# Optimization experiments

Measured on AMD Instinct MI355X. Metric: run time of the kernel, lower is better.

Reference implementation:

```python
import jax, jax.numpy as jnp
import numpy as np

N_NODES = 50000
N_EDGES = 800000
IN_DIM = 128
OUT_DIM = 128


def setup_inputs() -> dict:
    key = jax.random.key(0)
    k1, k2, k3, k4, k5, k6 = jax.random.split(key, 6)
    X = jax.random.normal(k1, (N_NODES, IN_DIM), dtype=jnp.float32)
    src = jax.random.randint(k2, (N_EDGES,), 0, N_NODES, dtype=jnp.int32)
    dst = jax.random.randint(k3, (N_EDGES,), 0, N_NODES, dtype=jnp.int32)
    # nn.Linear(in, out, bias=False) weight has shape (out, in)
    lim = 1.0 / np.sqrt(IN_DIM)
    W_self = jax.random.uniform(k4, (OUT_DIM, IN_DIM), dtype=jnp.float32, minval=-lim, maxval=lim)
    W_neigh = jax.random.uniform(k5, (OUT_DIM, IN_DIM), dtype=jnp.float32, minval=-lim, maxval=lim)
    bias = jnp.zeros((OUT_DIM,), dtype=jnp.float32)
    return {"X": X, "src": src, "dst": dst, "W_self": W_self, "W_neigh": W_neigh, "bias": bias}


def reference(X, src, dst, W_self, W_neigh, bias):
    # h_u = ReLU( W_self x_u + sum_{(v->u) in E} W_neigh x_v + bias )
    # Transform once per node (n_nodes x in_dim x out_dim GEMMs), then
    # gather transformed source features and scatter-add into destinations.
    h_self = jnp.einsum('ni,oi->no', X, W_self)        # [N, out]
    xw_neigh = jnp.einsum('ni,oi->no', X, W_neigh)     # [N, out]
    h_neigh = jax.ops.segment_sum(xw_neigh[src], dst, num_segments=N_NODES)
    return jax.nn.relu(h_self + h_neigh + bias)
```

## Files before the change

### kernel.cpp

```cpp
#include <hip/hip_runtime.h>

#define IN_DIM 128
#define OUT_DIM 128
#define BM 64
#define KT 32

typedef __attribute__((ext_vector_type(8))) short short8v;
typedef __attribute__((ext_vector_type(4))) float float4v;

__device__ __forceinline__ unsigned short bf16_hi(float x) {
    unsigned int u = __float_as_uint(x);
    return (unsigned short)((u + 0x7fffu + ((u >> 16) & 1u)) >> 16);
}
__device__ __forceinline__ float bf16_tof(unsigned short h) {
    return __uint_as_float(((unsigned int)h) << 16);
}

__global__ void scatter_kernel(const float* __restrict__ X,
                               const int* __restrict__ src,
                               const int* __restrict__ dst,
                               float* __restrict__ A,
                               int n_edges) {
    int gtid = blockIdx.x * blockDim.x + threadIdx.x;
    int e = gtid >> 5;
    if (e >= n_edges) return;
    int sub = gtid & 31;
    int s = src[e];
    int d = dst[e];
    const float4 v = *reinterpret_cast<const float4*>(
        X + (size_t)s * IN_DIM + sub * 4);
    float* o = A + (size_t)d * IN_DIM + sub * 4;
    unsafeAtomicAdd(o + 0, v.x);
    unsafeAtomicAdd(o + 1, v.y);
    unsafeAtomicAdd(o + 2, v.z);
    unsafeAtomicAdd(o + 3, v.w);
}

__global__ void hist_kernel(const int* __restrict__ dst, int* __restrict__ counts,
                            int n_edges) {
    int i = blockIdx.x * blockDim.x + threadIdx.x;
    int e0 = i * 4;
    if (e0 + 4 <= n_edges) {
        int4 d4 = *reinterpret_cast<const int4*>(dst + e0);
        atomicAdd(&counts[d4.x], 1);
        atomicAdd(&counts[d4.y], 1);
        atomicAdd(&counts[d4.z], 1);
        atomicAdd(&counts[d4.w], 1);
    } else {
        for (int e = e0; e < n_edges; ++e) atomicAdd(&counts[dst[e]], 1);
    }
}

__global__ __launch_bounds__(256)
void scan1_kernel(const int* __restrict__ counts, int* __restrict__ offs,
                  int* __restrict__ bsums, int n) {
    __shared__ int tmp[256];
    const int tid = threadIdx.x;
    const int i = blockIdx.x * 256 + tid;
    const int v = (i < n) ? counts[i] : 0;
    tmp[tid] = v;
    __syncthreads();
    #pragma unroll
    for (int d = 1; d < 256; d <<= 1) {
        int t = (tid >= d) ? tmp[tid - d] : 0;
        __syncthreads();
        tmp[tid] += t;
        __syncthreads();
    }
    if (i < n) offs[i] = tmp[tid] - v;
    if (tid == 255) bsums[blockIdx.x] = tmp[255];
}

__global__ __launch_bounds__(256)
void scan2_kernel(int* __restrict__ bsums, int nb) {
    __shared__ int tmp[256];
    __shared__ int carry;
    const int tid = threadIdx.x;
    if (tid == 0) carry = 0;
    __syncthreads();
    for (int base = 0; base < nb; base += 256) {
        const int i = base + tid;
        const int v = (i < nb) ? bsums[i] : 0;
        tmp[tid] = v;
        __syncthreads();
        #pragma unroll
        for (int d = 1; d < 256; d <<= 1) {
            int t = (tid >= d) ? tmp[tid - d] : 0;
            __syncthreads();
            tmp[tid] += t;
            __syncthreads();
        }
        if (i < nb) bsums[i] = carry + tmp[tid] - v;
        __syncthreads();
        if (tid == 0) carry += tmp[255];
        __syncthreads();
    }
}

__global__ __launch_bounds__(256)
void scan3_kernel(int* __restrict__ offs, const int* __restrict__ bsums,
                  int* __restrict__ cursor, int n) {
    const int i = blockIdx.x * 256 + threadIdx.x;
    if (i < n) {
        const int o = offs[i] + bsums[blockIdx.x];
        offs[i] = o;
        cursor[i] = o;
    }
}

__global__ void bucket_kernel(const int* __restrict__ src,
                              const int* __restrict__ dst,
                              int* __restrict__ cursor,
                              int* __restrict__ src_sorted, int n_edges) {
    int e = blockIdx.x * blockDim.x + threadIdx.x;
    if (e < n_edges) {
        const int pos = atomicAdd(&cursor[dst[e]], 1);
        src_sorted[pos] = src[e];
    }
}

__global__ __launch_bounds__(256)
void accum_split_kernel(const float* __restrict__ X,
                        const int* __restrict__ offs,
                        const int* __restrict__ src_sorted,
                        unsigned short* __restrict__ Ahi,
                        unsigned short* __restrict__ Alo,
                        int n_nodes, int n_edges) {
    const int tid = threadIdx.x;
    const int u = blockIdx.x * 8 + (tid >> 5);
    if (u >= n_nodes) return;
    const int sub = tid & 31;

    const int beg = offs[u];
    const int end = (u == n_nodes - 1) ? n_edges : offs[u + 1];

    float4 acc = make_float4(0.f, 0.f, 0.f, 0.f);
    int e = beg;
    for (; e + 4 <= end; e += 4) {
        const int s0 = src_sorted[e + 0];
        const int s1 = src_sorted[e + 1];
        const int s2 = src_sorted[e + 2];
        const int s3 = src_sorted[e + 3];
        const float4 v0 = *reinterpret_cast<const float4*>(X + (size_t)s0 * IN_DIM + sub * 4);
        const float4 v1 = *reinterpret_cast<const float4*>(X + (size_t)s1 * IN_DIM + sub * 4);
        const float4 v2 = *reinterpret_cast<const float4*>(X + (size_t)s2 * IN_DIM + sub * 4);
        const float4 v3 = *reinterpret_cast<const float4*>(X + (size_t)s3 * IN_DIM + sub * 4);
        acc.x += v0.x + v1.x + v2.x + v3.x;
        acc.y += v0.y + v1.y + v2.y + v3.y;
        acc.z += v0.z + v1.z + v2.z + v3.z;
        acc.w += v0.w + v1.w + v2.w + v3.w;
    }
    for (; e < end; ++e) {
        const int s = src_sorted[e];
        const float4 v = *reinterpret_cast<const float4*>(X + (size_t)s * IN_DIM + sub * 4);
        acc.x += v.x; acc.y += v.y; acc.z += v.z; acc.w += v.w;
    }

    ushort4 hi, lo;
    hi.x = bf16_hi(acc.x); lo.x = bf16_hi(acc.x - bf16_tof(hi.x));
    hi.y = bf16_hi(acc.y); lo.y = bf16_hi(acc.y - bf16_tof(hi.y));
    hi.z = bf16_hi(acc.z); lo.z = bf16_hi(acc.z - bf16_tof(hi.z));
    hi.w = bf16_hi(acc.w); lo.w = bf16_hi(acc.w - bf16_tof(hi.w));
    *reinterpret_cast<ushort4*>(Ahi + (size_t)u * IN_DIM + sub * 4) = hi;
    *reinterpret_cast<ushort4*>(Alo + (size_t)u * IN_DIM + sub * 4) = lo;
}

__global__ void xsplit_kernel(const float* __restrict__ X,
                              unsigned short* __restrict__ Xsp, int n_nodes) {
    int i = blockIdx.x * blockDim.x + threadIdx.x;
    if (i >= n_nodes * 32) return;
    const int node = i >> 5, g = i & 31;
    const float4 x = *reinterpret_cast<const float4*>(X + (size_t)node * IN_DIM + g * 4);
    ushort4 hi, lo;
    hi.x = bf16_hi(x.x); lo.x = bf16_hi(x.x - bf16_tof(hi.x));
    hi.y = bf16_hi(x.y); lo.y = bf16_hi(x.y - bf16_tof(hi.y));
    hi.z = bf16_hi(x.z); lo.z = bf16_hi(x.z - bf16_tof(hi.z));
    hi.w = bf16_hi(x.w); lo.w = bf16_hi(x.w - bf16_tof(hi.w));
    *reinterpret_cast<ushort4*>(Xsp + (size_t)node * 256 + g * 4) = hi;
    *reinterpret_cast<ushort4*>(Xsp + (size_t)node * 256 + 128 + g * 4) = lo;
}

__global__ void wsplit_kernel(const float* __restrict__ W1,
                              const float* __restrict__ W2,
                              unsigned short* __restrict__ W1h,
                              unsigned short* __restrict__ W1l,
                              unsigned short* __restrict__ W2h,
                              unsigned short* __restrict__ W2l) {
    int i = blockIdx.x * blockDim.x + threadIdx.x;
    if (i >= OUT_DIM * IN_DIM) return;
    float a = W1[i], b = W2[i];
    unsigned short ah = bf16_hi(a), bh = bf16_hi(b);
    W1h[i] = ah; W1l[i] = bf16_hi(a - bf16_tof(ah));
    W2h[i] = bh; W2l[i] = bf16_hi(b - bf16_tof(bh));
}

__global__ __launch_bounds__(256, 4)
void mfma_gemm_kernel(const unsigned short* Xsp,
                      const unsigned short* __restrict__ Ahi,
                      const unsigned short* __restrict__ Alo,
                      const unsigned short* __restrict__ W1h,
                      const unsigned short* __restrict__ W1l,
                      const unsigned short* __restrict__ W2h,
                      const unsigned short* __restrict__ W2l,
                      const float* __restrict__ bias,
                      float* out,
                      int n_nodes) {
    __shared__ unsigned short Fs[64 * 64];
    __shared__ unsigned short Ws[128 * 64];

    const int tid  = threadIdx.x;
    const int lane = tid & 63;
    const int wid  = tid >> 6;
    const int wm   = wid >> 1;
    const int wn   = wid & 1;
    const int lr   = lane & 15;
    const int lk   = lane >> 4;
    const int node0 = blockIdx.x * 64;

    const int fr = tid >> 3;
    const int c  = tid & 7;
    const int swz = (c ^ (fr & 7)) * 8;

    float4v acc[2][4];
    #pragma unroll
    for (int mi = 0; mi < 2; ++mi)
        #pragma unroll
        for (int ni = 0; ni < 4; ++ni) acc[mi][ni] = (float4v)0.f;

    const unsigned short* wseg[6] = {W1h, W1l, W1h, W2h, W2l, W2h};

    short8v fv[2], wv[4];

    {
        const int seg = 0, khalf = 0;
        #pragma unroll
        for (int j = 0; j < 2; ++j) {
            const int node = node0 + fr + j * 32;
            short8v v = (short8v)0;
            if (node < n_nodes)
                v = *reinterpret_cast<const short8v*>(
                    Xsp + (size_t)node * 256 + khalf + c * 8);
            fv[j] = v;
        }
        #pragma unroll
        for (int j = 0; j < 4; ++j)
            wv[j] = *reinterpret_cast<const short8v*>(
                wseg[seg] + (size_t)(fr + j * 32) * 128 + khalf + c * 8);
    }

    #pragma unroll
    for (int t = 0; t < 12; ++t) {
        __syncthreads();
        #pragma unroll
        for (int j = 0; j < 2; ++j)
            *reinterpret_cast<short8v*>(&Fs[(fr + j * 32) * 64 + swz]) = fv[j];
        #pragma unroll
        for (int j = 0; j < 4; ++j)
            *reinterpret_cast<short8v*>(&Ws[(fr + j * 32) * 64 + swz]) = wv[j];
        __syncthreads();

        if (t < 11) {
            const int tn = t + 1;
            const int seg = tn >> 1;
            const int khalf = (tn & 1) * 64;
            #pragma unroll
            for (int j = 0; j < 2; ++j) {
                const int node = node0 + fr + j * 32;
                short8v v = (short8v)0;
                if (node < n_nodes) {
                    if (seg < 3) {
                        v = *reinterpret_cast<const short8v*>(
                            Xsp + (size_t)node * 256 + (seg == 2 ? 128 : 0) +
                            khalf + c * 8);
                    } else {
                        const unsigned short* Ap = (seg == 5) ? Alo : Ahi;
                        v = *reinterpret_cast<const short8v*>(
                            Ap + (size_t)node * 128 + khalf + c * 8);
                    }
                }
                fv[j] = v;
            }
            #pragma unroll
            for (int j = 0; j < 4; ++j)
                wv[j] = *reinterpret_cast<const short8v*>(
                    wseg[seg] + (size_t)(fr + j * 32) * 128 + khalf + c * 8);
        }

        #pragma unroll
        for (int ks = 0; ks < 2; ++ks) {
            const int cc = ((ks * 4 + lk) ^ (lr & 7)) * 8;
            short8v a[2], b[4];
            #pragma unroll
            for (int mi = 0; mi < 2; ++mi) {
                const int row = wm * 32 + mi * 16 + lr;
                a[mi] = *reinterpret_cast<const short8v*>(&Fs[row * 64 + cc]);
            }
            #pragma unroll
            for (int ni = 0; ni < 4; ++ni) {
                const int o = wn * 64 + ni * 16 + lr;
                b[ni] = *reinterpret_cast<const short8v*>(&Ws[o * 64 + cc]);
            }
            #pragma unroll
            for (int mi = 0; mi < 2; ++mi)
                #pragma unroll
                for (int ni = 0; ni < 4; ++ni)
                    acc[mi][ni] = __builtin_amdgcn_mfma_f32_16x16x32_bf16(
                        a[mi], b[ni], acc[mi][ni], 0, 0, 0);
        }
    }

    #pragma unroll
    for (int ni = 0; ni < 4; ++ni) {
        const int o = wn * 64 + ni * 16 + lr;
        const float bo = bias[o];
        #pragma unroll
        for (int mi = 0; mi < 2; ++mi) {
            const int nodeb = node0 + wm * 32 + mi * 16 + lk * 4;
            #pragma unroll
            for (int r = 0; r < 4; ++r) {
                const int node = nodeb + r;
                if (node < n_nodes)
                    out[(size_t)node * OUT_DIM + o] =
                        fmaxf(acc[mi][ni][r] + bo, 0.f);
            }
        }
    }
}

__global__ __launch_bounds__(256)
void gemm_kernel(const float* __restrict__ X,
                 const float* __restrict__ A,
                 const float* __restrict__ Wself,
                 const float* __restrict__ Wneigh,
                 const float* __restrict__ bias,
                 float* __restrict__ out,
                 int n_nodes) {
    __shared__ alignas(16) float Wt[KT][132];
    __shared__ alignas(16) float Xs[BM][KT + 4];

    const int tid   = threadIdx.x;
    const int o_grp = tid & 31;
    const int n_grp = tid >> 5;
    const int node0 = blockIdx.x * BM;

    float acc[8][4];
    #pragma unroll
    for (int i = 0; i < 8; ++i)
        #pragma unroll
        for (int j = 0; j < 4; ++j) acc[i][j] = 0.f;

    for (int kt = 0; kt < 2 * IN_DIM; kt += KT) {
        const float* Wsrc = (kt < IN_DIM) ? Wself : Wneigh;
        const float* Fsrc = (kt < IN_DIM) ? X : A;
        const int kbase = kt & (IN_DIM - 1);
        __syncthreads();
        {
            const int k4 = tid & 7;
            int o = tid >> 3;
            #pragma unroll
            for (int p = 0; p < 4; ++p, o += 32) {
                float4 w = *reinterpret_cast<const float4*>(
                    Wsrc + o * IN_DIM + kbase + k4 * 4);
                Wt[k4 * 4 + 0][o] = w.x;
                Wt[k4 * 4 + 1][o] = w.y;
                Wt[k4 * 4 + 2][o] = w.z;
                Wt[k4 * 4 + 3][o] = w.w;
            }
        }
        {
            const int k4 = tid & 7;
            int n = tid >> 3;
            #pragma unroll
            for (int p = 0; p < 2; ++p, n += 32) {
                const int node = node0 + n;
                float4 x = make_float4(0.f, 0.f, 0.f, 0.f);
                if (node < n_nodes)
                    x = *reinterpret_cast<const float4*>(
                        Fsrc + (size_t)node * IN_DIM + kbase + k4 * 4);
                *reinterpret_cast<float4*>(&Xs[n][k4 * 4]) = x;
            }
        }
        __syncthreads();
        #pragma unroll
        for (int k4 = 0; k4 < KT; k4 += 4) {
            float4 w0 = *reinterpret_cast<const float4*>(&Wt[k4 + 0][o_grp * 4]);
            float4 w1 = *reinterpret_cast<const float4*>(&Wt[k4 + 1][o_grp * 4]);
            float4 w2 = *reinterpret_cast<const float4*>(&Wt[k4 + 2][o_grp * 4]);
            float4 w3 = *reinterpret_cast<const float4*>(&Wt[k4 + 3][o_grp * 4]);
            #pragma unroll
            for (int nn = 0; nn < 8; ++nn) {
                float4 x = *reinterpret_cast<const float4*>(
                    &Xs[n_grp * 8 + nn][k4]);
                acc[nn][0] = fmaf(x.x, w0.x, acc[nn][0]);
                acc[nn][0] = fmaf(x.y, w1.x, acc[nn][0]);
                acc[nn][0] = fmaf(x.z, w2.x, acc[nn][0]);
                acc[nn][0] = fmaf(x.w, w3.x, acc[nn][0]);
                acc[nn][1] = fmaf(x.x, w0.y, acc[nn][1]);
                acc[nn][1] = fmaf(x.y, w1.y, acc[nn][1]);
                acc[nn][1] = fmaf(x.z, w2.y, acc[nn][1]);
                acc[nn][1] = fmaf(x.w, w3.y, acc[nn][1]);
                acc[nn][2] = fmaf(x.x, w0.z, acc[nn][2]);
                acc[nn][2] = fmaf(x.y, w1.z, acc[nn][2]);
                acc[nn][2] = fmaf(x.z, w2.z, acc[nn][2]);
                acc[nn][2] = fmaf(x.w, w3.z, acc[nn][2]);
                acc[nn][3] = fmaf(x.x, w0.w, acc[nn][3]);
                acc[nn][3] = fmaf(x.y, w1.w, acc[nn][3]);
                acc[nn][3] = fmaf(x.z, w2.w, acc[nn][3]);
                acc[nn][3] = fmaf(x.w, w3.w, acc[nn][3]);
            }
        }
    }

    const float4 b = *reinterpret_cast<const float4*>(bias + o_grp * 4);
    #pragma unroll
    for (int nn = 0; nn < 8; ++nn) {
        const int node = node0 + n_grp * 8 + nn;
        if (node < n_nodes) {
            float4 r;
            r.x = fmaxf(acc[nn][0] + b.x, 0.f);
            r.y = fmaxf(acc[nn][1] + b.y, 0.f);
            r.z = fmaxf(acc[nn][2] + b.z, 0.f);
            r.w = fmaxf(acc[nn][3] + b.w, 0.f);
            *reinterpret_cast<float4*>(
                out + (size_t)node * OUT_DIM + o_grp * 4) = r;
        }
    }
}

extern "C" void kernel_launch(void* const* d_in, const int* in_sizes, int n_in,
                              void* d_out, int out_size, void* d_ws, size_t ws_size,
                              hipStream_t stream) {
    const float* X      = (const float*)d_in[0];
    const int*   src    = (const int*)d_in[1];
    const int*   dst    = (const int*)d_in[2];
    const float* Wself  = (const float*)d_in[3];
    const float* Wneigh = (const float*)d_in[4];
    const float* bias   = (const float*)d_in[5];
    float*       out    = (float*)d_out;

    const int n_nodes = in_sizes[0] / IN_DIM;
    const int n_edges = in_sizes[1];
    const int nb = (n_nodes + 255) / 256;

    char* w = (char*)d_ws;
    auto take = [&](size_t bytes) {
        char* p = w;
        w += (bytes + 15) & ~(size_t)15;
        return p;
    };
    unsigned short* Ahi = (unsigned short*)take((size_t)n_nodes * IN_DIM * 2);
    unsigned short* Alo = (unsigned short*)take((size_t)n_nodes * IN_DIM * 2);
    int* counts    = (int*)take((size_t)n_nodes * sizeof(int));
    int* offs      = (int*)take((size_t)n_nodes * sizeof(int));
    int* cursor    = (int*)take((size_t)n_nodes * sizeof(int));
    int* bsums     = (int*)take((size_t)nb * sizeof(int));
    int* srcsorted = (int*)take((size_t)n_edges * sizeof(int));
    unsigned short* W1h = (unsigned short*)take((size_t)OUT_DIM * IN_DIM * 2);
    unsigned short* W1l = (unsigned short*)take((size_t)OUT_DIM * IN_DIM * 2);
    unsigned short* W2h = (unsigned short*)take((size_t)OUT_DIM * IN_DIM * 2);
    unsigned short* W2l = (unsigned short*)take((size_t)OUT_DIM * IN_DIM * 2);
    const size_t needed = (size_t)(w - (char*)d_ws);

    const int eblocks = (n_edges + 255) / 256;

    if (needed <= ws_size) {
        hipMemsetAsync(counts, 0, (size_t)n_nodes * sizeof(int), stream);
        hist_kernel<<<(n_edges / 4 + 256) / 256 + 1, 256, 0, stream>>>(dst, counts, n_edges);
        scan1_kernel<<<nb, 256, 0, stream>>>(counts, offs, bsums, n_nodes);
        scan2_kernel<<<1, 256, 0, stream>>>(bsums, nb);
        scan3_kernel<<<nb, 256, 0, stream>>>(offs, bsums, cursor, n_nodes);
        bucket_kernel<<<eblocks, 256, 0, stream>>>(src, dst, cursor, srcsorted,
                                                   n_edges);
        unsigned short* Xsp = (unsigned short*)d_out;
        xsplit_kernel<<<(n_nodes * 32 + 255) / 256, 256, 0, stream>>>(X, Xsp, n_nodes);
        wsplit_kernel<<<(OUT_DIM * IN_DIM + 255) / 256, 256, 0, stream>>>(
            Wself, Wneigh, W1h, W1l, W2h, W2l);
        accum_split_kernel<<<(n_nodes + 7) / 8, 256, 0, stream>>>(
            X, offs, srcsorted, Ahi, Alo, n_nodes, n_edges);
        mfma_gemm_kernel<<<(n_nodes + 63) / 64, 256, 0, stream>>>(
            Xsp, Ahi, Alo, W1h, W1l, W2h, W2l, bias, out, n_nodes);
    } else {
        float* A = (float*)d_ws;
        hipMemsetAsync(A, 0, (size_t)n_nodes * IN_DIM * sizeof(float), stream);
        const long long sthreads = (long long)n_edges * 32;
        const int sblocks = (int)((sthreads + 255) / 256);
        scatter_kernel<<<sblocks, 256, 0, stream>>>(X, src, dst, A, n_edges);
        gemm_kernel<<<(n_nodes + BM - 1) / BM, 256, 0, stream>>>(
            X, A, Wself, Wneigh, bias, out, n_nodes);
    }
}
```

Measured before the change: 264.4 us.

## Fuse CSR build and neighbor aggregation into one cooperative persistent kernel

Merges the preprocessing pipeline into a single cooperatively launched persistent kernel separated by grid-wide syncs. It covers zeroing counts, splitting the weights and X into bf16 hi/lo, the histogram, the three-pass scan, bucketing by destination and the neighbor accumulation. This removes many separate kernel launches and the memset on the stream. The accumulation loop is also unrolled to eight edges with two accumulators for more memory-level parallelism. In exchange it relies on cooperative launch, pays for several grid.sync barriers, and runs the serial block-sum scan on one block while the rest of the grid waits; a multi-kernel fallback is kept.

```diff
diff --git a/kernel.cpp b/kernel.cpp
--- a/kernel.cpp
+++ b/kernel.cpp
@@ -1,4 +1,7 @@
 #include <hip/hip_runtime.h>
+#include <hip/hip_cooperative_groups.h>
+
+namespace cg = cooperative_groups;
 
 #define IN_DIM 128
 #define OUT_DIM 128
@@ -7,6 +10,7 @@
 
 typedef __attribute__((ext_vector_type(8))) short short8v;
 typedef __attribute__((ext_vector_type(4))) float float4v;
+typedef __attribute__((ext_vector_type(4))) float f4v;
 
 __device__ __forceinline__ unsigned short bf16_hi(float x) {
     unsigned int u = __float_as_uint(x);
@@ -14,6 +18,495 @@
 }
 __device__ __forceinline__ float bf16_tof(unsigned short h) {
     return __uint_as_float(((unsigned int)h) << 16);
+}
+
+__global__ __launch_bounds__(256, 4)
+void fused_all_kernel(const float* __restrict__ X,
+                      const int* __restrict__ src,
+                      const int* __restrict__ dst,
+                      const float* __restrict__ Wself,
+                      const float* __restrict__ Wneigh,
+                      int* __restrict__ counts,
+                      int* __restrict__ offs,
+                      int* __restrict__ cursor,
+                      int* __restrict__ bsums,
+                      int* __restrict__ srcsorted,
+                      unsigned short* __restrict__ Ahi,
+                      unsigned short* __restrict__ Alo,
+                      unsigned short* __restrict__ W1h,
+                      unsigned short* __restrict__ W1l,
+                      unsigned short* __restrict__ W2h,
+                      unsigned short* __restrict__ W2l,
+                      unsigned short* __restrict__ Xsp,
+                      int n_nodes, int n_edges, int nb) {
+    cg::grid_group grid = cg::this_grid();
+    __shared__ int tmp[256];
+    __shared__ int carry;
+
+    const int tid   = threadIdx.x;
+    const int gsize = gridDim.x * 256;
+    const int gtid  = blockIdx.x * 256 + tid;
+
+    for (int i = gtid; i < n_nodes; i += gsize) counts[i] = 0;
+    for (int i = gtid; i < OUT_DIM * IN_DIM; i += gsize) {
+        float a = Wself[i], b = Wneigh[i];
+        unsigned short ah = bf16_hi(a), bh = bf16_hi(b);
+        W1h[i] = ah; W1l[i] = bf16_hi(a - bf16_tof(ah));
+        W2h[i] = bh; W2l[i] = bf16_hi(b - bf16_tof(bh));
+    }
+    for (int i = gtid; i < n_nodes * 32; i += gsize) {
+        const int node = i >> 5, g = i & 31;
+        const float4 x = *reinterpret_cast<const float4*>(
+            X + (size_t)node * IN_DIM + g * 4);
+        ushort4 hi, lo;
+        hi.x = bf16_hi(x.x); lo.x = bf16_hi(x.x - bf16_tof(hi.x));
+        hi.y = bf16_hi(x.y); lo.y = bf16_hi(x.y - bf16_tof(hi.y));
+        hi.z = bf16_hi(x.z); lo.z = bf16_hi(x.z - bf16_tof(hi.z));
+        hi.w = bf16_hi(x.w); lo.w = bf16_hi(x.w - bf16_tof(hi.w));
+        *reinterpret_cast<ushort4*>(Xsp + (size_t)node * 256 + g * 4) = hi;
+        *reinterpret_cast<ushort4*>(Xsp + (size_t)node * 256 + 128 + g * 4) = lo;
+    }
+    grid.sync();
+
+    {
+        const int n4 = n_edges >> 2;
+        for (int i = gtid; i < n4; i += gsize) {
+            int4 d4 = reinterpret_cast<const int4*>(dst)[i];
+            atomicAdd(&counts[d4.x], 1);
+            atomicAdd(&counts[d4.y], 1);
+            atomicAdd(&counts[d4.z], 1);
+            atomicAdd(&counts[d4.w], 1);
+        }
+        for (int e = (n4 << 2) + gtid; e < n_edges; e += gsize)
+            atomicAdd(&counts[dst[e]], 1);
+    }
+    grid.sync();
+
+    for (int ci = blockIdx.x; ci < nb; ci += gridDim.x) {
+        const int i = ci * 256 + tid;
+        const int v = (i < n_nodes) ? counts[i] : 0;
+        tmp[tid] = v;
+        __syncthreads();
+        #pragma unroll
+        for (int d = 1; d < 256; d <<= 1) {
+            int t = (tid >= d) ? tmp[tid - d] : 0;
+            __syncthreads();
+            tmp[tid] += t;
+            __syncthreads();
+        }
+        if (i < n_nodes) offs[i] = tmp[tid] - v;
+        if (tid == 255) bsums[ci] = tmp[255];
+        __syncthreads();
+    }
+    grid.sync();
+
+    if (blockIdx.x == 0) {
+        if (tid == 0) carry = 0;
+        __syncthreads();
+        for (int base = 0; base < nb; base += 256) {
+            const int i = base + tid;
+            const int v = (i < nb) ? bsums[i] : 0;
+            tmp[tid] = v;
+            __syncthreads();
+            #pragma unroll
+            for (int d = 1; d < 256; d <<= 1) {
+                int t = (tid >= d) ? tmp[tid - d] : 0;
+                __syncthreads();
+                tmp[tid] += t;
+                __syncthreads();
+            }
+            if (i < nb) bsums[i] = carry + tmp[tid] - v;
+            __syncthreads();
+            if (tid == 0) carry += tmp[255];
+            __syncthreads();
+        }
+    }
+    grid.sync();
+
+    for (int i = gtid; i < n_nodes; i += gsize) {
+        const int o = offs[i] + bsums[i >> 8];
+        offs[i] = o;
+        cursor[i] = o;
+    }
+    grid.sync();
+
+    for (int e = gtid; e < n_edges; e += gsize) {
+        const int pos = atomicAdd(&cursor[dst[e]], 1);
+        srcsorted[pos] = src[e];
+    }
+    grid.sync();
+
+    {
+        const int sub  = tid & 31;
+        const int grp  = gtid >> 5;
+        const int ngrp = gsize >> 5;
+        for (int u = grp; u < n_nodes; u += ngrp) {
+            const int beg = offs[u];
+            const int end = (u == n_nodes - 1) ? n_edges : offs[u + 1];
+            f4v a0 = (f4v)0.f, a1 = (f4v)0.f;
+            int e = beg;
+            for (; e + 8 <= end; e += 8) {
+                const int s0 = srcsorted[e + 0];
+                const int s1 = srcsorted[e + 1];
+                const int s2 = srcsorted[e + 2];
+                const int s3 = srcsorted[e + 3];
+                const int s4 = srcsorted[e + 4];
+                const int s5 = srcsorted[e + 5];
+                const int s6 = srcsorted[e + 6];
+                const int s7 = srcsorted[e + 7];
+                f4v v0 = *reinterpret_cast<const f4v*>(X + (size_t)s0 * IN_DIM + sub * 4);
+                f4v v1 = *reinterpret_cast<const f4v*>(X + (size_t)s1 * IN_DIM + sub * 4);
+                f4v v2 = *reinterpret_cast<const f4v*>(X + (size_t)s2 * IN_DIM + sub * 4);
+                f4v v3 = *reinterpret_cast<const f4v*>(X + (size_t)s3 * IN_DIM + sub * 4);
+                f4v v4 = *reinterpret_cast<const f4v*>(X + (size_t)s4 * IN_DIM + sub * 4);
+                f4v v5 = *reinterpret_cast<const f4v*>(X + (size_t)s5 * IN_DIM + sub * 4);
+                f4v v6 = *reinterpret_cast<const f4v*>(X + (size_t)s6 * IN_DIM + sub * 4);
+                f4v v7 = *reinterpret_cast<const f4v*>(X + (size_t)s7 * IN_DIM + sub * 4);
+                a0 += v0 + v1 + v2 + v3;
+                a1 += v4 + v5 + v6 + v7;
+            }
+            for (; e + 4 <= end; e += 4) {
+                const int s0 = srcsorted[e + 0];
+                const int s1 = srcsorted[e + 1];
+                const int s2 = srcsorted[e + 2];
+                const int s3 = srcsorted[e + 3];
+                f4v v0 = *reinterpret_cast<const f4v*>(X + (size_t)s0 * IN_DIM + sub * 4);
+                f4v v1 = *reinterpret_cast<const f4v*>(X + (size_t)s1 * IN_DIM + sub * 4);
+                f4v v2 = *reinterpret_cast<const f4v*>(X + (size_t)s2 * IN_DIM + sub * 4);
+                f4v v3 = *reinterpret_cast<const f4v*>(X + (size_t)s3 * IN_DIM + sub * 4);
+                a0 += v0 + v1;
+                a1 += v2 + v3;
+            }
+            for (; e < end; ++e) {
+                const int s = srcsorted[e];
+                a0 += *reinterpret_cast<const f4v*>(X + (size_t)s * IN_DIM + sub * 4);
+            }
+            const f4v r = a0 + a1;
+            ushort4 hi, lo;
+            hi.x = bf16_hi(r.x); lo.x = bf16_hi(r.x - bf16_tof(hi.x));
+            hi.y = bf16_hi(r.y); lo.y = bf16_hi(r.y - bf16_tof(hi.y));
+            hi.z = bf16_hi(r.z); lo.z = bf16_hi(r.z - bf16_tof(hi.z));
+            hi.w = bf16_hi(r.w); lo.w = bf16_hi(r.w - bf16_tof(hi.w));
+            *reinterpret_cast<ushort4*>(Ahi + (size_t)u * IN_DIM + sub * 4) = hi;
+            *reinterpret_cast<ushort4*>(Alo + (size_t)u * IN_DIM + sub * 4) = lo;
+        }
+    }
+}
+
+__global__ __launch_bounds__(256)
+void prep_kernel(const float* __restrict__ X,
+                 const float* __restrict__ Wself,
+                 const float* __restrict__ Wneigh,
+                 int* __restrict__ counts,
+                 unsigned short* __restrict__ W1h,
+                 unsigned short* __restrict__ W1l,
+                 unsigned short* __restrict__ W2h,
+                 unsigned short* __restrict__ W2l,
+                 unsigned short* __restrict__ Xsp,
+                 int n_nodes) {
+    const int gtid  = blockIdx.x * 256 + threadIdx.x;
+    const int gsize = gridDim.x * 256;
+
+    for (int i = gtid; i < n_nodes; i += gsize) counts[i] = 0;
+
+    for (int i = gtid; i < OUT_DIM * IN_DIM; i += gsize) {
+        float a = Wself[i], b = Wneigh[i];
+        unsigned short ah = bf16_hi(a), bh = bf16_hi(b);
+        W1h[i] = ah; W1l[i] = bf16_hi(a - bf16_tof(ah));
+        W2h[i] = bh; W2l[i] = bf16_hi(b - bf16_tof(bh));
+    }
+
+    for (int i = gtid; i < n_nodes * 32; i += gsize) {
+        const int node = i >> 5, g = i & 31;
+        const float4 x = *reinterpret_cast<const float4*>(
+            X + (size_t)node * IN_DIM + g * 4);
+        ushort4 hi, lo;
+        hi.x = bf16_hi(x.x); lo.x = bf16_hi(x.x - bf16_tof(hi.x));
+        hi.y = bf16_hi(x.y); lo.y = bf16_hi(x.y - bf16_tof(hi.y));
+        hi.z = bf16_hi(x.z); lo.z = bf16_hi(x.z - bf16_tof(hi.z));
+        hi.w = bf16_hi(x.w); lo.w = bf16_hi(x.w - bf16_tof(hi.w));
+        *reinterpret_cast<ushort4*>(Xsp + (size_t)node * 256 + g * 4) = hi;
+        *reinterpret_cast<ushort4*>(Xsp + (size_t)node * 256 + 128 + g * 4) = lo;
+    }
+}
+
+__global__ void hist_kernel(const int* __restrict__ dst, int* __restrict__ counts,
+                            int n_edges) {
+    int i = blockIdx.x * blockDim.x + threadIdx.x;
+    int e0 = i * 4;
+    if (e0 + 4 <= n_edges) {
+        int4 d4 = *reinterpret_cast<const int4*>(dst + e0);
+        atomicAdd(&counts[d4.x], 1);
+        atomicAdd(&counts[d4.y], 1);
+        atomicAdd(&counts[d4.z], 1);
+        atomicAdd(&counts[d4.w], 1);
+    } else {
+        for (int e = e0; e < n_edges; ++e) atomicAdd(&counts[dst[e]], 1);
+    }
+}
+
+__global__ __launch_bounds__(256)
+void scan1_kernel(const int* __restrict__ counts, int* __restrict__ offs,
+                  int* __restrict__ bsums, int n) {
+    __shared__ int tmp[256];
+    const int tid = threadIdx.x;
+    const int i = blockIdx.x * 256 + tid;
+    const int v = (i < n) ? counts[i] : 0;
+    tmp[tid] = v;
+    __syncthreads();
+    #pragma unroll
+    for (int d = 1; d < 256; d <<= 1) {
+        int t = (tid >= d) ? tmp[tid - d] : 0;
+        __syncthreads();
+        tmp[tid] += t;
+        __syncthreads();
+    }
+    if (i < n) offs[i] = tmp[tid] - v;
+    if (tid == 255) bsums[blockIdx.x] = tmp[255];
+}
+
+__global__ __launch_bounds__(256)
+void scan2_kernel(int* __restrict__ bsums, int nb) {
+    __shared__ int tmp[256];
+    __shared__ int carry;
+    const int tid = threadIdx.x;
+    if (tid == 0) carry = 0;
+    __syncthreads();
+    for (int base = 0; base < nb; base += 256) {
+        const int i = base + tid;
+        const int v = (i < nb) ? bsums[i] : 0;
+        tmp[tid] = v;
+        __syncthreads();
+        #pragma unroll
+        for (int d = 1; d < 256; d <<= 1) {
+            int t = (tid >= d) ? tmp[tid - d] : 0;
+            __syncthreads();
+            tmp[tid] += t;
+            __syncthreads();
+        }
+        if (i < nb) bsums[i] = carry + tmp[tid] - v;
+        __syncthreads();
+        if (tid == 0) carry += tmp[255];
+        __syncthreads();
+    }
+}
+
+__global__ __launch_bounds__(256)
+void scan3_kernel(int* __restrict__ offs, const int* __restrict__ bsums,
+                  int* __restrict__ cursor, int n) {
+    const int i = blockIdx.x * 256 + threadIdx.x;
+    if (i < n) {
+        const int o = offs[i] + bsums[blockIdx.x];
+        offs[i] = o;
+        cursor[i] = o;
+    }
+}
+
+__global__ void bucket_kernel(const int* __restrict__ src,
+                              const int* __restrict__ dst,
+                              int* __restrict__ cursor,
+                              int* __restrict__ src_sorted, int n_edges) {
+    int e = blockIdx.x * blockDim.x + threadIdx.x;
+    if (e < n_edges) {
+        const int pos = atomicAdd(&cursor[dst[e]], 1);
+        src_sorted[pos] = src[e];
+    }
+}
+
+__global__ __launch_bounds__(256)
+void accum8_kernel(const float* __restrict__ X,
+                   const int* __restrict__ offs,
+                   const int* __restrict__ src_sorted,
+                   unsigned short* __restrict__ Ahi,
+                   unsigned short* __restrict__ Alo,
+                   int n_nodes, int n_edges) {
+    const int tid   = threadIdx.x;
+    const int sub   = tid & 31;
+    const int grp   = (blockIdx.x * 256 + tid) >> 5;
+    const int ngrp  = (gridDim.x * 256) >> 5;
+    for (int u = grp; u < n_nodes; u += ngrp) {
+        const int beg = offs[u];
+        const int end = (u == n_nodes - 1) ? n_edges : offs[u + 1];
+        f4v a0 = (f4v)0.f, a1 = (f4v)0.f;
+        int e = beg;
+        for (; e + 8 <= end; e += 8) {
+            const int s0 = src_sorted[e + 0];
+            const int s1 = src_sorted[e + 1];
+            const int s2 = src_sorted[e + 2];
+            const int s3 = src_sorted[e + 3];
+            const int s4 = src_sorted[e + 4];
+            const int s5 = src_sorted[e + 5];
+            const int s6 = src_sorted[e + 6];
+            const int s7 = src_sorted[e + 7];
+            f4v v0 = *reinterpret_cast<const f4v*>(X + (size_t)s0 * IN_DIM + sub * 4);
+            f4v v1 = *reinterpret_cast<const f4v*>(X + (size_t)s1 * IN_DIM + sub * 4);
+            f4v v2 = *reinterpret_cast<const f4v*>(X + (size_t)s2 * IN_DIM + sub * 4);
+            f4v v3 = *reinterpret_cast<const f4v*>(X + (size_t)s3 * IN_DIM + sub * 4);
+            f4v v4 = *reinterpret_cast<const f4v*>(X + (size_t)s4 * IN_DIM + sub * 4);
+            f4v v5 = *reinterpret_cast<const f4v*>(X + (size_t)s5 * IN_DIM + sub * 4);
+            f4v v6 = *reinterpret_cast<const f4v*>(X + (size_t)s6 * IN_DIM + sub * 4);
+            f4v v7 = *reinterpret_cast<const f4v*>(X + (size_t)s7 * IN_DIM + sub * 4);
+            a0 += v0 + v1 + v2 + v3;
+            a1 += v4 + v5 + v6 + v7;
+        }
+        for (; e + 4 <= end; e += 4) {
+            const int s0 = src_sorted[e + 0];
+            const int s1 = src_sorted[e + 1];
+            const int s2 = src_sorted[e + 2];
+            const int s3 = src_sorted[e + 3];
+            f4v v0 = *reinterpret_cast<const f4v*>(X + (size_t)s0 * IN_DIM + sub * 4);
+            f4v v1 = *reinterpret_cast<const f4v*>(X + (size_t)s1 * IN_DIM + sub * 4);
+            f4v v2 = *reinterpret_cast<const f4v*>(X + (size_t)s2 * IN_DIM + sub * 4);
+            f4v v3 = *reinterpret_cast<const f4v*>(X + (size_t)s3 * IN_DIM + sub * 4);
+            a0 += v0 + v1;
+            a1 += v2 + v3;
+        }
+        for (; e < end; ++e) {
+            const int s = src_sorted[e];
+            a0 += *reinterpret_cast<const f4v*>(X + (size_t)s * IN_DIM + sub * 4);
+        }
+        const f4v r = a0 + a1;
+        ushort4 hi, lo;
+        hi.x = bf16_hi(r.x); lo.x = bf16_hi(r.x - bf16_tof(hi.x));
+        hi.y = bf16_hi(r.y); lo.y = bf16_hi(r.y - bf16_tof(hi.y));
+        hi.z = bf16_hi(r.z); lo.z = bf16_hi(r.z - bf16_tof(hi.z));
+        hi.w = bf16_hi(r.w); lo.w = bf16_hi(r.w - bf16_tof(hi.w));
+        *reinterpret_cast<ushort4*>(Ahi + (size_t)u * IN_DIM + sub * 4) = hi;
+        *reinterpret_cast<ushort4*>(Alo + (size_t)u * IN_DIM + sub * 4) = lo;
+    }
+}
+
+__global__ __launch_bounds__(256, 4)
+void mfma_gemm_kernel(const unsigned short* Xsp,
+                      const unsigned short* __restrict__ Ahi,
+                      const unsigned short* __restrict__ Alo,
+                      const unsigned short* __restrict__ W1h,
+                      const unsigned short* __restrict__ W1l,
+                      const unsigned short* __restrict__ W2h,
+                      const unsigned short* __restrict__ W2l,
+                      const float* __restrict__ bias,
+                      float* out,
+                      int n_nodes) {
+    __shared__ unsigned short Fs[64 * 64];
+    __shared__ unsigned short Ws[128 * 64];
+
+    const int tid  = threadIdx.x;
+    const int lane = tid & 63;
+    const int wid  = tid >> 6;
+    const int wm   = wid >> 1;
+    const int wn   = wid & 1;
+    const int lr   = lane & 15;
+    const int lk   = lane >> 4;
+    const int node0 = blockIdx.x * 64;
+
+    const int fr = tid >> 3;
+    const int c  = tid & 7;
+    const int swz = (c ^ (fr & 7)) * 8;
+
+    float4v acc[2][4];
+    #pragma unroll
+    for (int mi = 0; mi < 2; ++mi)
+        #pragma unroll
+        for (int ni = 0; ni < 4; ++ni) acc[mi][ni] = (float4v)0.f;
+
+    const unsigned short* wseg[6] = {W1h, W1l, W1h, W2h, W2l, W2h};
+
+    short8v fv[2], wv[4];
+
+    {
+        const int khalf = 0;
+        #pragma unroll
+        for (int j = 0; j < 2; ++j) {
+            const int node = node0 + fr + j * 32;
+            short8v v = (short8v)0;
+            if (node < n_nodes)
+                v = *reinterpret_cast<const short8v*>(
+                    Xsp + (size_t)node * 256 + khalf + c * 8);
+            fv[j] = v;
+        }
+        #pragma unroll
+        for (int j = 0; j < 4; ++j)
+            wv[j] = *reinterpret_cast<const short8v*>(
+                wseg[0] + (size_t)(fr + j * 32) * 128 + khalf + c * 8);
+    }
+
+    #pragma unroll
+    for (int t = 0; t < 12; ++t) {
+        __syncthreads();
+        #pragma unroll
+        for (int j = 0; j < 2; ++j)
+            *reinterpret_cast<short8v*>(&Fs[(fr + j * 32) * 64 + swz]) = fv[j];
+        #pragma unroll
+        for (int j = 0; j < 4; ++j)
+            *reinterpret_cast<short8v*>(&Ws[(fr + j * 32) * 64 + swz]) = wv[j];
+        __syncthreads();
+
+        if (t < 11) {
+            const int tn = t + 1;
+            const int seg = tn >> 1;
+            const int khalf = (tn & 1) * 64;
+            #pragma unroll
+            for (int j = 0; j < 2; ++j) {
+                const int node = node0 + fr + j * 32;
+                short8v v = (short8v)0;
+                if (node < n_nodes) {
+                    if (seg < 3) {
+                        v = *reinterpret_cast<const short8v*>(
+                            Xsp + (size_t)node * 256 + (seg == 2 ? 128 : 0) +
+                            khalf + c * 8);
+                    } else {
+                        const unsigned short* Ap = (seg == 5) ? Alo : Ahi;
+                        v = *reinterpret_cast<const short8v*>(
+                            Ap + (size_t)node * 128 + khalf + c * 8);
+                    }
+                }
+                fv[j] = v;
+            }
+            #pragma unroll
+            for (int j = 0; j < 4; ++j)
+                wv[j] = *reinterpret_cast<const short8v*>(
+                    wseg[seg] + (size_t)(fr + j * 32) * 128 + khalf + c * 8);
+        }
+
+        #pragma unroll
+        for (int ks = 0; ks < 2; ++ks) {
+            const int cc = ((ks * 4 + lk) ^ (lr & 7)) * 8;
+            short8v a[2], b[4];
+            #pragma unroll
+            for (int mi = 0; mi < 2; ++mi) {
+                const int row = wm * 32 + mi * 16 + lr;
+                a[mi] = *reinterpret_cast<const short8v*>(&Fs[row * 64 + cc]);
+            }
+            #pragma unroll
+            for (int ni = 0; ni < 4; ++ni) {
+                const int o = wn * 64 + ni * 16 + lr;
+                b[ni] = *reinterpret_cast<const short8v*>(&Ws[o * 64 + cc]);
+            }
+            #pragma unroll
+            for (int mi = 0; mi < 2; ++mi)
+                #pragma unroll
+                for (int ni = 0; ni < 4; ++ni)
+                    acc[mi][ni] = __builtin_amdgcn_mfma_f32_16x16x32_bf16(
+                        a[mi], b[ni], acc[mi][ni], 0, 0, 0);
+        }
+    }
+
+    #pragma unroll
+    for (int ni = 0; ni < 4; ++ni) {
+        const int o = wn * 64 + ni * 16 + lr;
+        const float bo = bias[o];
+        #pragma unroll
+        for (int mi = 0; mi < 2; ++mi) {
+            const int nodeb = node0 + wm * 32 + mi * 16 + lk * 4;
+            #pragma unroll
+            for (int r = 0; r < 4; ++r) {
+                const int node = nodeb + r;
+                if (node < n_nodes)
+                    out[(size_t)node * OUT_DIM + o] =
+                        fmaxf(acc[mi][ni][r] + bo, 0.f);
+            }
+        }
+    }
 }
 
 __global__ void scatter_kernel(const float* __restrict__ X,
@@ -36,297 +529,6 @@
     unsafeAtomicAdd(o + 3, v.w);
 }
 
-__global__ void hist_kernel(const int* __restrict__ dst, int* __restrict__ counts,
-                            int n_edges) {
-    int i = blockIdx.x * blockDim.x + threadIdx.x;
-    int e0 = i * 4;
-    if (e0 + 4 <= n_edges) {
-        int4 d4 = *reinterpret_cast<const int4*>(dst + e0);
-        atomicAdd(&counts[d4.x], 1);
-        atomicAdd(&counts[d4.y], 1);
-        atomicAdd(&counts[d4.z], 1);
-        atomicAdd(&counts[d4.w], 1);
-    } else {
-        for (int e = e0; e < n_edges; ++e) atomicAdd(&counts[dst[e]], 1);
-    }
-}
-
-__global__ __launch_bounds__(256)
-void scan1_kernel(const int* __restrict__ counts, int* __restrict__ offs,
-                  int* __restrict__ bsums, int n) {
-    __shared__ int tmp[256];
-    const int tid = threadIdx.x;
-    const int i = blockIdx.x * 256 + tid;
-    const int v = (i < n) ? counts[i] : 0;
-    tmp[tid] = v;
-    __syncthreads();
-    #pragma unroll
-    for (int d = 1; d < 256; d <<= 1) {
-        int t = (tid >= d) ? tmp[tid - d] : 0;
-        __syncthreads();
-        tmp[tid] += t;
-        __syncthreads();
-    }
-    if (i < n) offs[i] = tmp[tid] - v;
-    if (tid == 255) bsums[blockIdx.x] = tmp[255];
-}
-
-__global__ __launch_bounds__(256)
-void scan2_kernel(int* __restrict__ bsums, int nb) {
-    __shared__ int tmp[256];
-    __shared__ int carry;
-    const int tid = threadIdx.x;
-    if (tid == 0) carry = 0;
-    __syncthreads();
-    for (int base = 0; base < nb; base += 256) {
-        const int i = base + tid;
-        const int v = (i < nb) ? bsums[i] : 0;
-        tmp[tid] = v;
-        __syncthreads();
-        #pragma unroll
-        for (int d = 1; d < 256; d <<= 1) {
-            int t = (tid >= d) ? tmp[tid - d] : 0;
-            __syncthreads();
-            tmp[tid] += t;
-            __syncthreads();
-        }
-        if (i < nb) bsums[i] = carry + tmp[tid] - v;
-        __syncthreads();
-        if (tid == 0) carry += tmp[255];
-        __syncthreads();
-    }
-}
-
-__global__ __launch_bounds__(256)
-void scan3_kernel(int* __restrict__ offs, const int* __restrict__ bsums,
-                  int* __restrict__ cursor, int n) {
-    const int i = blockIdx.x * 256 + threadIdx.x;
-    if (i < n) {
-        const int o = offs[i] + bsums[blockIdx.x];
-        offs[i] = o;
-        cursor[i] = o;
-    }
-}
-
-__global__ void bucket_kernel(const int* __restrict__ src,
-                              const int* __restrict__ dst,
-                              int* __restrict__ cursor,
-                              int* __restrict__ src_sorted, int n_edges) {
-    int e = blockIdx.x * blockDim.x + threadIdx.x;
-    if (e < n_edges) {
-        const int pos = atomicAdd(&cursor[dst[e]], 1);
-        src_sorted[pos] = src[e];
-    }
-}
-
-__global__ __launch_bounds__(256)
-void accum_split_kernel(const float* __restrict__ X,
-                        const int* __restrict__ offs,
-                        const int* __restrict__ src_sorted,
-                        unsigned short* __restrict__ Ahi,
-                        unsigned short* __restrict__ Alo,
-                        int n_nodes, int n_edges) {
-    const int tid = threadIdx.x;
-    const int u = blockIdx.x * 8 + (tid >> 5);
-    if (u >= n_nodes) return;
-    const int sub = tid & 31;
-
-    const int beg = offs[u];
-    const int end = (u == n_nodes - 1) ? n_edges : offs[u + 1];
-
-    float4 acc = make_float4(0.f, 0.f, 0.f, 0.f);
-    int e = beg;
-    for (; e + 4 <= end; e += 4) {
-        const int s0 = src_sorted[e + 0];
-        const int s1 = src_sorted[e + 1];
-        const int s2 = src_sorted[e + 2];
-        const int s3 = src_sorted[e + 3];
-        const float4 v0 = *reinterpret_cast<const float4*>(X + (size_t)s0 * IN_DIM + sub * 4);
-        const float4 v1 = *reinterpret_cast<const float4*>(X + (size_t)s1 * IN_DIM + sub * 4);
-        const float4 v2 = *reinterpret_cast<const float4*>(X + (size_t)s2 * IN_DIM + sub * 4);
-        const float4 v3 = *reinterpret_cast<const float4*>(X + (size_t)s3 * IN_DIM + sub * 4);
-        acc.x += v0.x + v1.x + v2.x + v3.x;
-        acc.y += v0.y + v1.y + v2.y + v3.y;
-        acc.z += v0.z + v1.z + v2.z + v3.z;
-        acc.w += v0.w + v1.w + v2.w + v3.w;
-    }
-    for (; e < end; ++e) {
-        const int s = src_sorted[e];
-        const float4 v = *reinterpret_cast<const float4*>(X + (size_t)s * IN_DIM + sub * 4);
-        acc.x += v.x; acc.y += v.y; acc.z += v.z; acc.w += v.w;
-    }
-
-    ushort4 hi, lo;
-    hi.x = bf16_hi(acc.x); lo.x = bf16_hi(acc.x - bf16_tof(hi.x));
-    hi.y = bf16_hi(acc.y); lo.y = bf16_hi(acc.y - bf16_tof(hi.y));
-    hi.z = bf16_hi(acc.z); lo.z = bf16_hi(acc.z - bf16_tof(hi.z));
-    hi.w = bf16_hi(acc.w); lo.w = bf16_hi(acc.w - bf16_tof(hi.w));
-    *reinterpret_cast<ushort4*>(Ahi + (size_t)u * IN_DIM + sub * 4) = hi;
-    *reinterpret_cast<ushort4*>(Alo + (size_t)u * IN_DIM + sub * 4) = lo;
-}
-
-__global__ void xsplit_kernel(const float* __restrict__ X,
-                              unsigned short* __restrict__ Xsp, int n_nodes) {
-    int i = blockIdx.x * blockDim.x + threadIdx.x;
-    if (i >= n_nodes * 32) return;
-    const int node = i >> 5, g = i & 31;
-    const float4 x = *reinterpret_cast<const float4*>(X + (size_t)node * IN_DIM + g * 4);
-    ushort4 hi, lo;
-    hi.x = bf16_hi(x.x); lo.x = bf16_hi(x.x - bf16_tof(hi.x));
-    hi.y = bf16_hi(x.y); lo.y = bf16_hi(x.y - bf16_tof(hi.y));
-    hi.z = bf16_hi(x.z); lo.z = bf16_hi(x.z - bf16_tof(hi.z));
-    hi.w = bf16_hi(x.w); lo.w = bf16_hi(x.w - bf16_tof(hi.w));
-    *reinterpret_cast<ushort4*>(Xsp + (size_t)node * 256 + g * 4) = hi;
-    *reinterpret_cast<ushort4*>(Xsp + (size_t)node * 256 + 128 + g * 4) = lo;
-}
-
-__global__ void wsplit_kernel(const float* __restrict__ W1,
-                              const float* __restrict__ W2,
-                              unsigned short* __restrict__ W1h,
-                              unsigned short* __restrict__ W1l,
-                              unsigned short* __restrict__ W2h,
-                              unsigned short* __restrict__ W2l) {
-    int i = blockIdx.x * blockDim.x + threadIdx.x;
-    if (i >= OUT_DIM * IN_DIM) return;
-    float a = W1[i], b = W2[i];
-    unsigned short ah = bf16_hi(a), bh = bf16_hi(b);
-    W1h[i] = ah; W1l[i] = bf16_hi(a - bf16_tof(ah));
-    W2h[i] = bh; W2l[i] = bf16_hi(b - bf16_tof(bh));
-}
-
-__global__ __launch_bounds__(256, 4)
-void mfma_gemm_kernel(const unsigned short* Xsp,
-                      const unsigned short* __restrict__ Ahi,
-                      const unsigned short* __restrict__ Alo,
-                      const unsigned short* __restrict__ W1h,
-                      const unsigned short* __restrict__ W1l,
-                      const unsigned short* __restrict__ W2h,
-                      const unsigned short* __restrict__ W2l,
-                      const float* __restrict__ bias,
-                      float* out,
-                      int n_nodes) {
-    __shared__ unsigned short Fs[64 * 64];
-    __shared__ unsigned short Ws[128 * 64];
-
-    const int tid  = threadIdx.x;
-    const int lane = tid & 63;
-    const int wid  = tid >> 6;
-    const int wm   = wid >> 1;
-    const int wn   = wid & 1;
-    const int lr   = lane & 15;
-    const int lk   = lane >> 4;
-    const int node0 = blockIdx.x * 64;
-
-    const int fr = tid >> 3;
-    const int c  = tid & 7;
-    const int swz = (c ^ (fr & 7)) * 8;
-
-    float4v acc[2][4];
-    #pragma unroll
-    for (int mi = 0; mi < 2; ++mi)
-        #pragma unroll
-        for (int ni = 0; ni < 4; ++ni) acc[mi][ni] = (float4v)0.f;
-
-    const unsigned short* wseg[6] = {W1h, W1l, W1h, W2h, W2l, W2h};
-
-    short8v fv[2], wv[4];
-
-    {
-        const int seg = 0, khalf = 0;
-        #pragma unroll
-        for (int j = 0; j < 2; ++j) {
-            const int node = node0 + fr + j * 32;
-            short8v v = (short8v)0;
-            if (node < n_nodes)
-                v = *reinterpret_cast<const short8v*>(
-                    Xsp + (size_t)node * 256 + khalf + c * 8);
-            fv[j] = v;
-        }
-        #pragma unroll
-        for (int j = 0; j < 4; ++j)
-            wv[j] = *reinterpret_cast<const short8v*>(
-                wseg[seg] + (size_t)(fr + j * 32) * 128 + khalf + c * 8);
-    }
-
-    #pragma unroll
-    for (int t = 0; t < 12; ++t) {
-        __syncthreads();
-        #pragma unroll
-        for (int j = 0; j < 2; ++j)
-            *reinterpret_cast<short8v*>(&Fs[(fr + j * 32) * 64 + swz]) = fv[j];
-        #pragma unroll
-        for (int j = 0; j < 4; ++j)
-            *reinterpret_cast<short8v*>(&Ws[(fr + j * 32) * 64 + swz]) = wv[j];
-        __syncthreads();
-
-        if (t < 11) {
-            const int tn = t + 1;
-            const int seg = tn >> 1;
-            const int khalf = (tn & 1) * 64;
-            #pragma unroll
-            for (int j = 0; j < 2; ++j) {
-                const int node = node0 + fr + j * 32;
-                short8v v = (short8v)0;
-                if (node < n_nodes) {
-                    if (seg < 3) {
-                        v = *reinterpret_cast<const short8v*>(
-                            Xsp + (size_t)node * 256 + (seg == 2 ? 128 : 0) +
-                            khalf + c * 8);
-                    } else {
-                        const unsigned short* Ap = (seg == 5) ? Alo : Ahi;
-                        v = *reinterpret_cast<const short8v*>(
-                            Ap + (size_t)node * 128 + khalf + c * 8);
-                    }
-                }
-                fv[j] = v;
-            }
-            #pragma unroll
-            for (int j = 0; j < 4; ++j)
-                wv[j] = *reinterpret_cast<const short8v*>(
-                    wseg[seg] + (size_t)(fr + j * 32) * 128 + khalf + c * 8);
-        }
-
-        #pragma unroll
-        for (int ks = 0; ks < 2; ++ks) {
-            const int cc = ((ks * 4 + lk) ^ (lr & 7)) * 8;
-            short8v a[2], b[4];
-            #pragma unroll
-            for (int mi = 0; mi < 2; ++mi) {
-                const int row = wm * 32 + mi * 16 + lr;
-                a[mi] = *reinterpret_cast<const short8v*>(&Fs[row * 64 + cc]);
-            }
-            #pragma unroll
-            for (int ni = 0; ni < 4; ++ni) {
-                const int o = wn * 64 + ni * 16 + lr;
-                b[ni] = *reinterpret_cast<const short8v*>(&Ws[o * 64 + cc]);
-            }
-            #pragma unroll
-            for (int mi = 0; mi < 2; ++mi)
-                #pragma unroll
-                for (int ni = 0; ni < 4; ++ni)
-                    acc[mi][ni] = __builtin_amdgcn_mfma_f32_16x16x32_bf16(
-                        a[mi], b[ni], acc[mi][ni], 0, 0, 0);
-        }
-    }
-
-    #pragma unroll
-    for (int ni = 0; ni < 4; ++ni) {
-        const int o = wn * 64 + ni * 16 + lr;
-        const float bo = bias[o];
-        #pragma unroll
-        for (int mi = 0; mi < 2; ++mi) {
-            const int nodeb = node0 + wm * 32 + mi * 16 + lk * 4;
-            #pragma unroll
-            for (int r = 0; r < 4; ++r) {
-                const int node = nodeb + r;
-                if (node < n_nodes)
-                    out[(size_t)node * OUT_DIM + o] =
-                        fmaxf(acc[mi][ni][r] + bo, 0.f);
-            }
-        }
-    }
-}
-
 __global__ __launch_bounds__(256)
 void gemm_kernel(const float* __restrict__ X,
                  const float* __restrict__ A,
@@ -337,18 +539,15 @@
                  int n_nodes) {
     __shared__ alignas(16) float Wt[KT][132];
     __shared__ alignas(16) float Xs[BM][KT + 4];
-
     const int tid   = threadIdx.x;
     const int o_grp = tid & 31;
     const int n_grp = tid >> 5;
     const int node0 = blockIdx.x * BM;
-
     float acc[8][4];
     #pragma unroll
     for (int i = 0; i < 8; ++i)
         #pragma unroll
         for (int j = 0; j < 4; ++j) acc[i][j] = 0.f;
-
     for (int kt = 0; kt < 2 * IN_DIM; kt += KT) {
         const float* Wsrc = (kt < IN_DIM) ? Wself : Wneigh;
         const float* Fsrc = (kt < IN_DIM) ? X : A;
@@ -410,7 +609,6 @@
             }
         }
     }
-
     const float4 b = *reinterpret_cast<const float4*>(bias + o_grp * 4);
     #pragma unroll
     for (int nn = 0; nn < 8; ++nn) {
@@ -438,9 +636,9 @@
     const float* bias   = (const float*)d_in[5];
     float*       out    = (float*)d_out;
 
-    const int n_nodes = in_sizes[0] / IN_DIM;
-    const int n_edges = in_sizes[1];
-    const int nb = (n_nodes + 255) / 256;
+    int n_nodes = in_sizes[0] / IN_DIM;
+    int n_edges = in_sizes[1];
+    int nb = (n_nodes + 255) / 256;
 
     char* w = (char*)d_ws;
     auto take = [&](size_t bytes) {
@@ -461,31 +659,53 @@
     unsigned short* W2l = (unsigned short*)take((size_t)OUT_DIM * IN_DIM * 2);
     const size_t needed = (size_t)(w - (char*)d_ws);
 
-    const int eblocks = (n_edges + 255) / 256;
-
     if (needed <= ws_size) {
-        hipMemsetAsync(counts, 0, (size_t)n_nodes * sizeof(int), stream);
-        hist_kernel<<<(n_edges / 4 + 256) / 256 + 1, 256, 0, stream>>>(dst, counts, n_edges);
-        scan1_kernel<<<nb, 256, 0, stream>>>(counts, offs, bsums, n_nodes);
-        scan2_kernel<<<1, 256, 0, stream>>>(bsums, nb);
-        scan3_kernel<<<nb, 256, 0, stream>>>(offs, bsums, cursor, n_nodes);
-        bucket_kernel<<<eblocks, 256, 0, stream>>>(src, dst, cursor, srcsorted,
-                                                   n_edges);
         unsigned short* Xsp = (unsigned short*)d_out;
-        xsplit_kernel<<<(n_nodes * 32 + 255) / 256, 256, 0, stream>>>(X, Xsp, n_nodes);
-        wsplit_kernel<<<(OUT_DIM * IN_DIM + 255) / 256, 256, 0, stream>>>(
-            Wself, Wneigh, W1h, W1l, W2h, W2l);
-        accum_split_kernel<<<(n_nodes + 7) / 8, 256, 0, stream>>>(
-            X, offs, srcsorted, Ahi, Alo, n_nodes, n_edges);
+
+        bool coop_ok = false;
+        int maxb = 0;
+        hipError_t oerr = hipOccupancyMaxActiveBlocksPerMultiprocessor(
+            &maxb, (const void*)fused_all_kernel, 256, 0);
+        if (oerr == hipSuccess && maxb > 0) {
+            int grid = maxb * 256;
+            if (grid > 1024) grid = 1024;
+            void* args[] = {(void*)&X, (void*)&src, (void*)&dst,
+                            (void*)&Wself, (void*)&Wneigh,
+                            (void*)&counts, (void*)&offs, (void*)&cursor,
+                            (void*)&bsums, (void*)&srcsorted,
+                            (void*)&Ahi, (void*)&Alo,
+                            (void*)&W1h, (void*)&W1l, (void*)&W2h, (void*)&W2l,
+                            (void*)&Xsp,
+                            (void*)&n_nodes, (void*)&n_edges, (void*)&nb};
+            hipError_t cerr = hipLaunchCooperativeKernel(
+                (void*)fused_all_kernel, dim3(grid), dim3(256), args, 0, stream);
+            coop_ok = (cerr == hipSuccess);
+        }
+
+        if (!coop_ok) {
+            const int eblocks = (n_edges + 255) / 256;
+            prep_kernel<<<2048, 256, 0, stream>>>(
+                X, Wself, Wneigh, counts, W1h, W1l, W2h, W2l, Xsp, n_nodes);
+            hist_kernel<<<(n_edges / 4 + 256) / 256 + 1, 256, 0, stream>>>(
+                dst, counts, n_edges);
+            scan1_kernel<<<nb, 256, 0, stream>>>(counts, offs, bsums, n_nodes);
+            scan2_kernel<<<1, 256, 0, stream>>>(bsums, nb);
+            scan3_kernel<<<nb, 256, 0, stream>>>(offs, bsums, cursor, n_nodes);
+            bucket_kernel<<<eblocks, 256, 0, stream>>>(src, dst, cursor,
+                                                       srcsorted, n_edges);
+            accum8_kernel<<<2048, 256, 0, stream>>>(
+                X, offs, srcsorted, Ahi, Alo, n_nodes, n_edges);
+        }
+
         mfma_gemm_kernel<<<(n_nodes + 63) / 64, 256, 0, stream>>>(
             Xsp, Ahi, Alo, W1h, W1l, W2h, W2l, bias, out, n_nodes);
     } else {
-        float* A = (float*)d_ws;
-        hipMemsetAsync(A, 0, (size_t)n_nodes * IN_DIM * sizeof(float), stream);
+        float* Af = (float*)d_ws;
+        hipMemsetAsync(Af, 0, (size_t)n_nodes * IN_DIM * sizeof(float), stream);
         const long long sthreads = (long long)n_edges * 32;
         const int sblocks = (int)((sthreads + 255) / 256);
-        scatter_kernel<<<sblocks, 256, 0, stream>>>(X, src, dst, A, n_edges);
+        scatter_kernel<<<sblocks, 256, 0, stream>>>(X, src, dst, Af, n_edges);
         gemm_kernel<<<(n_nodes + BM - 1) / BM, 256, 0, stream>>>(
-            X, A, Wself, Wneigh, bias, out, n_nodes);
-    }
-}
+            X, Af, Wself, Wneigh, bias, out, n_nodes);
+    }
+}
```

After: 759.1 us. +187.1%, slower.
